# Performance work log

Hardware: AMD Instinct MI355X
Metric: run time of the kernel (lower is better)

The kernel has to match this reference:

```python
import jax, jax.numpy as jnp
import numpy as np

N_NODES = 100000
N_EDGES = 6400000
HID = 32


def setup_inputs() -> dict:
    key = jax.random.key(0)
    ks = jax.random.split(key, 24)
    inp = {
        "x_G": jax.random.normal(ks[0], (N_NODES, 1), dtype=jnp.float32),
        "edge_index_G": jax.random.randint(ks[1], (2, N_EDGES), 0, N_NODES, dtype=jnp.int32),
        "x_H": jax.random.normal(ks[2], (N_NODES, 1), dtype=jnp.float32),
        "edge_index_H": jax.random.randint(ks[3], (2, N_EDGES), 0, N_NODES, dtype=jnp.int32),
    }
    ki = 4
    for i in range(3):
        d_in = 1 if i == 0 else HID
        inp[f"W1_{i}"] = jax.random.normal(ks[ki], (d_in, HID), dtype=jnp.float32) / np.sqrt(d_in); ki += 1
        inp[f"b1_{i}"] = jnp.zeros((HID,), dtype=jnp.float32)
        inp[f"W2_{i}"] = jax.random.normal(ks[ki], (HID, HID), dtype=jnp.float32) / np.sqrt(HID); ki += 1
        inp[f"b2_{i}"] = jnp.zeros((HID,), dtype=jnp.float32)
    inp["Wc1"] = jax.random.normal(ks[ki], (2 * HID, HID), dtype=jnp.float32) / np.sqrt(2 * HID); ki += 1
    inp["bc1"] = jnp.zeros((HID,), dtype=jnp.float32)
    inp["Wc2"] = jax.random.normal(ks[ki], (HID, 1), dtype=jnp.float32) / np.sqrt(HID); ki += 1
    inp["bc2"] = jnp.zeros((1,), dtype=jnp.float32)
    return inp


def _encode(x, edge_index, layers):
    n = x.shape[0]
    src, dst = edge_index[0], edge_index[1]
    for (W1, b1, W2, b2) in layers:
        # GIN aggregation: sum of neighbor messages scattered to targets; eps = 0
        agg = jax.ops.segment_sum(x[src], dst, num_segments=n)  # [N, d]
        h = x + agg  # (1 + eps) * x + agg with eps = 0
        h = jax.nn.relu(h @ W1 + b1) @ W2 + b2  # GIN MLP
        x = jax.nn.relu(h)  # outer F.relu in encode loop
    return jnp.sum(x, axis=0, keepdims=True)  # global_add_pool, single graph -> [1, HID]


def reference(x_G, edge_index_G, x_H, edge_index_H,
              W1_0, b1_0, W2_0, b2_0,
              W1_1, b1_1, W2_1, b2_1,
              W1_2, b1_2, W2_2, b2_2,
              Wc1, bc1, Wc2, bc2):
    layers = [(W1_0, b1_0, W2_0, b2_0),
              (W1_1, b1_1, W2_1, b2_1),
              (W1_2, b1_2, W2_2, b2_2)]
    h_G = _encode(x_G, edge_index_G, layers)
    h_H = _encode(x_H, edge_index_H, layers)
    combined = jnp.concatenate([h_G, h_H], axis=1)  # [1, 2*HID]
    out = jax.nn.relu(combined @ Wc1 + bc1) @ Wc2 + bc2
    return jax.nn.sigmoid(out)
```

## Files before the change

### kernel.cpp

```cpp
#include <hip/hip_runtime.h>
#include <hip/hip_bf16.h>
#include <math.h>
#include <string.h>

#define HID 32
#define PSHIFT 8
#define NPB (1 << PSHIFT)
#define MAXP 512
#define SLOTS 17408
#define SBITS 3
#define SBINS (1 << SBITS)
#define NBINS (NPB * SBINS)
#define GS 32
#define HS_ROWS 32
#define COLBUF 3072
#define COLBUF0 6144
#define EPB 16384
typedef unsigned short u16;
typedef unsigned char u8;

__device__ inline float e42f(unsigned b) {
    unsigned u = (b & 0x7fu) << 20;
    float f; memcpy(&f, &u, 4);
    return f * 0x1p120f;
}
__device__ inline unsigned f2e4(float f) {
    f = fminf(f, 448.f);
    float y = f * 0x1p-120f;
    unsigned r; memcpy(&r, &y, 4);
    r = r + 0x7FFFFu + ((r >> 20) & 1u);
    return (r >> 20) & 0x7fu;
}
__device__ inline void acc_e4(float* a, unsigned w) {
    a[0] += e42f(w);
    a[1] += e42f(w >> 8);
    a[2] += e42f(w >> 16);
    a[3] += e42f(w >> 24);
}

__global__ void zero_kernel(float* __restrict__ p, int n) {
    int i = blockIdx.x * blockDim.x + threadIdx.x;
    if (i < n) p[i] = 0.f;
}
__global__ void init_gcur(int* __restrict__ gcur, int P) {
    int b = blockIdx.x * blockDim.x + threadIdx.x;
    if (b < P) gcur[b * GS] = b * SLOTS;
}

__global__ void partition_edges(const int* __restrict__ src, const int* __restrict__ dst,
                                int* __restrict__ gcur, unsigned* __restrict__ staged,
                                int E, int P) {
    __shared__ int hc[4][MAXP];
    __shared__ int hbase[MAXP];
    __shared__ int cur[MAXP];
    __shared__ int run[MAXP];
    __shared__ unsigned sortedv[4096];
    __shared__ u16 bktid[4096];
    __shared__ int wsums[4];
    __shared__ int sTotal;
    int t = threadIdx.x, wid = t >> 6, lane = t & 63;
    for (int i = t; i < 4 * MAXP; i += 256) (&hc[0][0])[i] = 0;
    __syncthreads();

    int base = blockIdx.x * EPB;

    {
        int cbase = base + wid * 4096;
#pragma unroll
        for (int k = 0; k < 16; k++) {
            int e = cbase + k * 256 + lane * 4;
            int4 D;
            if (e + 3 < E) {
                D = *(const int4*)(dst + e);
            } else {
                int d0[4];
                for (int j = 0; j < 4; j++) d0[j] = (e + j < E) ? dst[e + j] : -1;
                D = make_int4(d0[0], d0[1], d0[2], d0[3]);
            }
            if (D.x >= 0) atomicAdd(&hc[wid][D.x >> PSHIFT], 1);
            if (D.y >= 0) atomicAdd(&hc[wid][D.y >> PSHIFT], 1);
            if (D.z >= 0) atomicAdd(&hc[wid][D.z >> PSHIFT], 1);
            if (D.w >= 0) atomicAdd(&hc[wid][D.w >> PSHIFT], 1);
        }
    }
    __syncthreads();

    int b0 = 2 * t, b1 = 2 * t + 1;
    int tot0 = 0, tot1 = 0;
    if (b0 < P) tot0 = hc[0][b0] + hc[1][b0] + hc[2][b0] + hc[3][b0];
    if (b1 < P) tot1 = hc[0][b1] + hc[1][b1] + hc[2][b1] + hc[3][b1];
    if (b0 < P && tot0) run[b0] = atomicAdd(&gcur[b0 * GS], tot0);
    if (b1 < P && tot1) run[b1] = atomicAdd(&gcur[b1 * GS], tot1);

    for (int c = 0; c < 4; c++) {
        int t0 = (b0 < P) ? hc[c][b0] : 0;
        int t1 = (b1 < P) ? hc[c][b1] : 0;
        int s = t0 + t1;
        int incl = s;
#pragma unroll
        for (int off = 1; off < 64; off <<= 1) {
            int u = __shfl_up(incl, off, 64);
            if (lane >= off) incl += u;
        }
        if (lane == 63) wsums[wid] = incl;
        __syncthreads();
        int woff = 0;
#pragma unroll
        for (int w = 0; w < 4; w++) if (w < wid) woff += wsums[w];
        int excl = woff + incl - s;
        if (b0 < P) { hbase[b0] = excl;      cur[b0] = excl; }
        if (b1 < P) { hbase[b1] = excl + t0; cur[b1] = excl + t0; }
        if (t == 255) sTotal = excl + s;
        __syncthreads();

#pragma unroll
        for (int r = 0; r < 4; r++) {
            int e = base + c * 4096 + r * 1024 + t * 4;
            int4 S4, D4;
            if (e + 3 < E) {
                S4 = *(const int4*)(src + e);
                D4 = *(const int4*)(dst + e);
            } else {
                int s0[4], d0[4];
                for (int j = 0; j < 4; j++) {
                    int ee = e + j;
                    s0[j] = (ee < E) ? src[ee] : -1;
                    d0[j] = (ee < E) ? dst[ee] : -1;
                }
                S4 = make_int4(s0[0], s0[1], s0[2], s0[3]);
                D4 = make_int4(d0[0], d0[1], d0[2], d0[3]);
            }
            int ss[4] = { S4.x, S4.y, S4.z, S4.w };
            int dd[4] = { D4.x, D4.y, D4.z, D4.w };
#pragma unroll
            for (int j = 0; j < 4; j++) {
                int d = dd[j];
                if (d >= 0) {
                    int bk = d >> PSHIFT;
                    int pos = atomicAdd(&cur[bk], 1);
                    sortedv[pos] = ((unsigned)(d & (NPB - 1)) << 17) | (unsigned)ss[j];
                    bktid[pos]   = (u16)bk;
                }
            }
        }
        __syncthreads();

        int total = sTotal;
        for (int i = t; i < total; i += 256) {
            int bk = bktid[i];
            int addr = run[bk] + (i - hbase[bk]);
            if (addr < (bk + 1) * SLOTS)
                staged[addr] = sortedv[i];
        }
        __syncthreads();

        if (c < 3) {
            if (b0 < P && t0) run[b0] += t0;
            if (b1 < P && t1) run[b1] += t1;
        }
    }
}

__global__ void scan_buckets(const int* __restrict__ gcur, int* __restrict__ colbase,
                             int* __restrict__ rowptr, int P, int N) {
    __shared__ int wsums[4];
    int t = threadIdx.x, wid = t >> 6, lane = t & 63;
    int b0 = 2 * t, b1 = 2 * t + 1;
    int c0 = 0, c1 = 0;
    if (b0 < P) { c0 = gcur[b0 * GS] - b0 * SLOTS; if (c0 > SLOTS) c0 = SLOTS; }
    if (b1 < P) { c1 = gcur[b1 * GS] - b1 * SLOTS; if (c1 > SLOTS) c1 = SLOTS; }
    int s = c0 + c1;
    int incl = s;
#pragma unroll
    for (int off = 1; off < 64; off <<= 1) {
        int u = __shfl_up(incl, off, 64);
        if (lane >= off) incl += u;
    }
    if (lane == 63) wsums[wid] = incl;
    __syncthreads();
    int woff = 0;
#pragma unroll
    for (int w = 0; w < 4; w++) if (w < wid) woff += wsums[w];
    int excl = woff + incl - s;
    if (b0 < P) colbase[b0] = excl;
    if (b1 < P) colbase[b1] = excl + c0;
    if (t == 255) {
        colbase[P] = excl + s;
        rowptr[N]  = excl + s;
    }
}

__global__ void sort_bucket(const unsigned* __restrict__ staged, const int* __restrict__ gcur,
                            const int* __restrict__ colbase,
                            int* __restrict__ rowptr, int* __restrict__ col, int N) {
    __shared__ int cnt[NBINS];
    __shared__ int wsum[4];
    __shared__ int sorted[SLOTS];
    int b = blockIdx.x;
    int t = threadIdx.x;
    int lane = t & 63, wid = t >> 6;
    int sBeg = b * SLOTS;
    int sEnd = gcur[b * GS]; if (sEnd > sBeg + SLOTS) sEnd = sBeg + SLOTS;
    int total = sEnd - sBeg;
    int colStart = colbase[b];
    int nodeBase = b << PSHIFT;

    for (int i = t; i < NBINS; i += 256) cnt[i] = 0;
    __syncthreads();
    for (int i = sBeg + t; i < sEnd; i += 256) {
        unsigned w = staged[i];
        int key = (int)((w >> 17) << SBITS) | (int)((w & 0x1FFFFu) >> 14);
        atomicAdd(&cnt[key], 1);
    }
    __syncthreads();

    int loc[SBINS]; int tot = 0;
#pragma unroll
    for (int k = 0; k < SBINS; k++) { loc[k] = tot; tot += cnt[(t << SBITS) + k]; }
    int incl = tot;
#pragma unroll
    for (int off = 1; off < 64; off <<= 1) {
        int u = __shfl_up(incl, off, 64);
        if (lane >= off) incl += u;
    }
    if (lane == 63) wsum[wid] = incl;
    __syncthreads();
    int woff = 0;
#pragma unroll
    for (int w = 0; w < 4; w++) if (w < wid) woff += wsum[w];
    int excl = woff + incl - tot;
    int node = nodeBase + t;
    if (node < N) rowptr[node] = colStart + excl;
#pragma unroll
    for (int k = 0; k < SBINS; k++) cnt[(t << SBITS) + k] = excl + loc[k];
    __syncthreads();

    for (int i = sBeg + t; i < sEnd; i += 256) {
        unsigned w = staged[i];
        int key = (int)((w >> 17) << SBITS) | (int)((w & 0x1FFFFu) >> 14);
        int pos = atomicAdd(&cnt[key], 1);
        sorted[pos] = (int)(w & 0x1FFFFu);
    }
    __syncthreads();
    for (int i = t; i < total; i += 256)
        col[colStart + i] = sorted[i];
}

__global__ void mlp0_fused(const int* __restrict__ rowptr, const int* __restrict__ col,
                           const float* __restrict__ x0,
                           const float* __restrict__ W1, const float* __restrict__ b1,
                           const float* __restrict__ W2, const float* __restrict__ b2,
                           u8* __restrict__ out, int n) {
    __shared__ float sW1[HID], sb1[HID], sW2[HID * HID], sb2[HID];
    __shared__ int colbuf[COLBUF0];
    int t = threadIdx.x;
    if (t < HID) { sW1[t] = W1[t]; sb1[t] = b1[t]; sb2[t] = b2[t]; }
    for (int i = t; i < HID * HID; i += blockDim.x) sW2[i] = W2[i];

    int firstNode = blockIdx.x * 64;
    int lastNode  = firstNode + 64; if (lastNode > n) lastNode = n;
    int blockStart = (firstNode < n) ? rowptr[firstNode] : 0;
    int blockEnd   = (firstNode < n) ? rowptr[lastNode] : 0;
    int stagedCnt = blockEnd - blockStart; if (stagedCnt > COLBUF0) stagedCnt = COLBUF0;
    for (int i = t; i < stagedCnt; i += 256) colbuf[i] = col[blockStart + i];
    __syncthreads();

    int node = firstNode + (t >> 2);
    int q    = t & 3;
    int lane = t & 63;
    int base = lane & ~3;
    bool active = node < n;

    float s = 0.f;
    if (active) {
        int beg = rowptr[node], end = rowptr[node + 1];
        int jSplit = blockStart + stagedCnt; if (jSplit > end) jSplit = end;
        int j = beg + q;
        for (; j + 12 < jSplit; j += 16) {
            int c0 = colbuf[j - blockStart];
            int c1 = colbuf[j + 4 - blockStart];
            int c2 = colbuf[j + 8 - blockStart];
            int c3 = colbuf[j + 12 - blockStart];
            s += x0[c0]; s += x0[c1]; s += x0[c2]; s += x0[c3];
        }
        for (; j < jSplit; j += 4) s += x0[colbuf[j - blockStart]];
        for (; j < end; j += 4) s += x0[col[j]];
    }
    s += __shfl_xor(s, 1, 64);
    s += __shfl_xor(s, 2, 64);
    float v = active ? (x0[node] + s) : 0.f;

    float h[8];
#pragma unroll
    for (int i = 0; i < 8; i++) h[i] = fmaxf(fmaf(v, sW1[q * 8 + i], sb1[q * 8 + i]), 0.f);
    float o[8];
#pragma unroll
    for (int i = 0; i < 8; i++) o[i] = sb2[q * 8 + i];
#pragma unroll
    for (int k = 0; k < HID; k++) {
        float hk = __shfl(h[k & 7], base | (k >> 3), 64);
#pragma unroll
        for (int i = 0; i < 8; i++) o[i] = fmaf(hk, sW2[k * HID + q * 8 + i], o[i]);
    }
    if (active) {
        unsigned w0 = f2e4(fmaxf(o[0], 0.f)) | (f2e4(fmaxf(o[1], 0.f)) << 8)
                    | (f2e4(fmaxf(o[2], 0.f)) << 16) | (f2e4(fmaxf(o[3], 0.f)) << 24);
        unsigned w1 = f2e4(fmaxf(o[4], 0.f)) | (f2e4(fmaxf(o[5], 0.f)) << 8)
                    | (f2e4(fmaxf(o[6], 0.f)) << 16) | (f2e4(fmaxf(o[7], 0.f)) << 24);
        uint2 pk = make_uint2(w0, w1);
        *(uint2*)(out + ((size_t)node << 5) + (q << 3)) = pk;
    }
}

template <bool REDUCE>
__global__ void mlp_fused(const int* __restrict__ rowptr, const int* __restrict__ col,
                          const u8* __restrict__ xin,
                          const float* __restrict__ W1, const float* __restrict__ b1,
                          const float* __restrict__ W2, const float* __restrict__ b2,
                          u8* __restrict__ xout, float* __restrict__ hsum, int n) {
    __shared__ float sW1[HID * HID], sb1[HID], sW2[HID * HID], sb2[HID];
    __shared__ int colbuf[COLBUF];
    __shared__ float red[4][HID];
    int t = threadIdx.x;
    for (int i = t; i < HID * HID; i += blockDim.x) { sW1[i] = W1[i]; sW2[i] = W2[i]; }
    if (t < HID) { sb1[t] = b1[t]; sb2[t] = b2[t]; }

    int firstNode = blockIdx.x * 32;
    int lastNode  = firstNode + 32; if (lastNode > n) lastNode = n;
    int blockStart = (firstNode < n) ? rowptr[firstNode] : 0;
    int blockEnd   = (firstNode < n) ? rowptr[lastNode] : 0;
    int stagedCnt = blockEnd - blockStart; if (stagedCnt > COLBUF) stagedCnt = COLBUF;
    for (int i = t; i < stagedCnt; i += 256) colbuf[i] = col[blockStart + i];
    __syncthreads();

    int node = firstNode + (t >> 3);
    int q    = t & 7;
    int lane = t & 63;
    int base = lane & ~7;
    bool active = node < n;

    float va[4];
#pragma unroll
    for (int i = 0; i < 4; i++) va[i] = 0.f;
    if (active) {
        int beg = rowptr[node], end = rowptr[node + 1];
        const u8* xq = xin + (q << 2);
        float a0[4], a1[4], a2[4], a3[4];
#pragma unroll
        for (int i = 0; i < 4; i++) a0[i] = a1[i] = a2[i] = a3[i] = 0.f;
        {
            unsigned w = *(const unsigned*)(xq + ((size_t)node << 5));
            acc_e4(a0, w);
        }
        int jSplit = blockStart + stagedCnt; if (jSplit > end) jSplit = end;
        int j = beg;
        for (; j + 8 <= jSplit; j += 8) {
            int lj = j - blockStart;
            int c0 = colbuf[lj+0], c1 = colbuf[lj+1], c2 = colbuf[lj+2], c3 = colbuf[lj+3];
            int c4 = colbuf[lj+4], c5 = colbuf[lj+5], c6 = colbuf[lj+6], c7 = colbuf[lj+7];
            unsigned w0 = *(const unsigned*)(xq + ((size_t)c0 << 5));
            unsigned w1 = *(const unsigned*)(xq + ((size_t)c1 << 5));
            unsigned w2 = *(const unsigned*)(xq + ((size_t)c2 << 5));
            unsigned w3 = *(const unsigned*)(xq + ((size_t)c3 << 5));
            unsigned w4 = *(const unsigned*)(xq + ((size_t)c4 << 5));
            unsigned w5 = *(const unsigned*)(xq + ((size_t)c5 << 5));
            unsigned w6 = *(const unsigned*)(xq + ((size_t)c6 << 5));
            unsigned w7 = *(const unsigned*)(xq + ((size_t)c7 << 5));
            acc_e4(a0, w0); acc_e4(a1, w1); acc_e4(a2, w2); acc_e4(a3, w3);
            acc_e4(a0, w4); acc_e4(a1, w5); acc_e4(a2, w6); acc_e4(a3, w7);
        }
        for (; j < jSplit; j++) {
            unsigned w = *(const unsigned*)(xq + ((size_t)colbuf[j - blockStart] << 5));
            acc_e4(a0, w);
        }
        for (; j < end; j++) {
            unsigned w = *(const unsigned*)(xq + ((size_t)col[j] << 5));
            acc_e4(a0, w);
        }
#pragma unroll
        for (int i = 0; i < 4; i++) va[i] = (a0[i] + a1[i]) + (a2[i] + a3[i]);
    }

    float h[4];
#pragma unroll
    for (int i = 0; i < 4; i++) h[i] = sb1[q * 4 + i];
#pragma unroll
    for (int k = 0; k < HID; k++) {
        float vk = __shfl(va[k & 3], base | (k >> 2), 64);
#pragma unroll
        for (int i = 0; i < 4; i++) h[i] = fmaf(vk, sW1[k * HID + q * 4 + i], h[i]);
    }
#pragma unroll
    for (int i = 0; i < 4; i++) h[i] = fmaxf(h[i], 0.f);

    float o[4];
#pragma unroll
    for (int i = 0; i < 4; i++) o[i] = sb2[q * 4 + i];
#pragma unroll
    for (int k = 0; k < HID; k++) {
        float hk = __shfl(h[k & 3], base | (k >> 2), 64);
#pragma unroll
        for (int i = 0; i < 4; i++) o[i] = fmaf(hk, sW2[k * HID + q * 4 + i], o[i]);
    }
#pragma unroll
    for (int i = 0; i < 4; i++) o[i] = fmaxf(o[i], 0.f);

    if (REDUCE) {
        if (!active) {
#pragma unroll
            for (int i = 0; i < 4; i++) o[i] = 0.f;
        }
#pragma unroll
        for (int i = 0; i < 4; i++) {
            float v = o[i];
            v += __shfl_xor(v, 8, 64);
            v += __shfl_xor(v, 16, 64);
            v += __shfl_xor(v, 32, 64);
            o[i] = v;
        }
        int wid = t >> 6;
        if (lane < 8) {
#pragma unroll
            for (int i = 0; i < 4; i++) red[wid][lane * 4 + i] = o[i];
        }
        __syncthreads();
        if (t < HID) {
            float s = red[0][t] + red[1][t] + red[2][t] + red[3][t];
            atomicAdd(&hsum[(blockIdx.x & (HS_ROWS - 1)) * (2 * HID) + t], s);
        }
    } else if (active) {
        unsigned pw = f2e4(o[0]) | (f2e4(o[1]) << 8) | (f2e4(o[2]) << 16) | (f2e4(o[3]) << 24);
        *(unsigned*)(xout + ((size_t)node << 5) + (q << 2)) = pw;
    }
}

__global__ void head_kernel(const float* __restrict__ hsumP,
                            const float* __restrict__ Wc1, const float* __restrict__ bc1,
                            const float* __restrict__ Wc2, const float* __restrict__ bc2,
                            float* __restrict__ out) {
    __shared__ float hs[2 * HID];
    int t = threadIdx.x;
    if (t < 2 * HID) {
        float s = 0.f;
        for (int r = 0; r < HS_ROWS; r++) s += hsumP[r * (2 * HID) + t];
        hs[t] = s;
    }
    __syncthreads();
    float val = 0.f;
    if (t < HID) {
        float acc = bc1[t];
        for (int i = 0; i < 2 * HID; i++) acc = fmaf(hs[i], Wc1[i * HID + t], acc);
        val = fmaxf(acc, 0.f) * Wc2[t];
    }
    for (int off = 32; off >= 1; off >>= 1) val += __shfl_xor(val, off, 64);
    if (t == 0) out[0] = 1.f / (1.f + expf(-(val + bc2[0])));
}

extern "C" void kernel_launch(void* const* d_in, const int* in_sizes, int n_in,
                              void* d_out, int out_size, void* d_ws, size_t ws_size,
                              hipStream_t stream) {
    const float* xg[2] = { (const float*)d_in[0], (const float*)d_in[2] };
    const int*   eg[2] = { (const int*)d_in[1],   (const int*)d_in[3] };
    const float* W1[3] = { (const float*)d_in[4], (const float*)d_in[8],  (const float*)d_in[12] };
    const float* b1[3] = { (const float*)d_in[5], (const float*)d_in[9],  (const float*)d_in[13] };
    const float* W2[3] = { (const float*)d_in[6], (const float*)d_in[10], (const float*)d_in[14] };
    const float* b2[3] = { (const float*)d_in[7], (const float*)d_in[11], (const float*)d_in[15] };
    const float* Wc1 = (const float*)d_in[16];
    const float* bc1 = (const float*)d_in[17];
    const float* Wc2 = (const float*)d_in[18];
    const float* bc2 = (const float*)d_in[19];

    const int N = in_sizes[0];
    const int E = in_sizes[1] / 2;
    const int P = (N + NPB - 1) >> PSHIFT;

    u8*       B0      = (u8*)d_ws;
    u8*       B1      = B0 + (size_t)N * 32;
    float*    hsumP   = (float*)(B1 + (size_t)N * 32);
    int*      rowptr  = (int*)(hsumP + HS_ROWS * 2 * HID);
    int*      col     = rowptr + (N + 1);
    int*      colbase = col + (size_t)E;
    int*      gcur    = colbase + (P + 1);
    unsigned* staged  = (unsigned*)(gcur + (size_t)P * GS);

    const int TB = 256;
    dim3 blk(TB);
    int gE16k = (E + EPB - 1) / EPB;
    int gN64 = (N + 63) / 64;
    int gN8  = (N + 31) / 32;
    int gP   = (P + TB - 1) / TB;

    zero_kernel<<<(HS_ROWS * 2 * HID + 255) / 256, 256, 0, stream>>>(hsumP, HS_ROWS * 2 * HID);

    for (int g = 0; g < 2; g++) {
        const float* x0  = xg[g];
        const int*   src = eg[g];
        const int*   dst = src + E;

        init_gcur<<<gP, blk, 0, stream>>>(gcur, P);
        partition_edges<<<gE16k, blk, 0, stream>>>(src, dst, gcur, staged, E, P);
        scan_buckets<<<1, blk, 0, stream>>>(gcur, colbase, rowptr, P, N);
        sort_bucket<<<P, blk, 0, stream>>>(staged, gcur, colbase, rowptr, col, N);

        mlp0_fused<<<gN64, blk, 0, stream>>>(rowptr, col, x0, W1[0], b1[0], W2[0], b2[0], B0, N);

        mlp_fused<false><<<gN8, blk, 0, stream>>>(rowptr, col, B0, W1[1], b1[1], W2[1], b2[1],
                                                  B1, nullptr, N);

        mlp_fused<true><<<gN8, blk, 0, stream>>>(rowptr, col, B1, W1[2], b1[2], W2[2], b2[2],
                                                 nullptr, hsumP + g * HID, N);
    }

    head_kernel<<<1, 64, 0, stream>>>(hsumP, Wc1, bc1, Wc2, bc2, (float*)d_out);
}
```

Before: 586.6 us.

## Use hardware FP8 convert builtins and halve edges per partition block

Replaces the software E4M3 encode/decode bit manipulation with the packed hardware conversion builtins (cvt_pk_f32_fp8 / cvt_pk_fp8_f32) when available, which shortens the inner gather-accumulate loops and output packing. Separately, it halves the edges handled per partition block (each wave-pair now shares one sorting pass, two passes instead of four), doubling the partition grid size. The hardware converter may round and handle saturation or NaN slightly differently from the software path, and more blocks means more global atomics on the bucket cursors.

```diff
diff --git a/kernel.cpp b/kernel.cpp
--- a/kernel.cpp
+++ b/kernel.cpp
@@ -15,16 +15,17 @@
 #define HS_ROWS 32
 #define COLBUF 3072
 #define COLBUF0 6144
-#define EPB 16384
+#define EPB 8192
 typedef unsigned short u16;
 typedef unsigned char u8;
-
-__device__ inline float e42f(unsigned b) {
+typedef float f32x2 __attribute__((ext_vector_type(2)));
+
+__device__ inline float e42f_sw(unsigned b) {
     unsigned u = (b & 0x7fu) << 20;
     float f; memcpy(&f, &u, 4);
     return f * 0x1p120f;
 }
-__device__ inline unsigned f2e4(float f) {
+__device__ inline unsigned f2e4_sw(float f) {
     f = fminf(f, 448.f);
     float y = f * 0x1p-120f;
     unsigned r; memcpy(&r, &y, 4);
@@ -32,10 +33,27 @@
     return (r >> 20) & 0x7fu;
 }
 __device__ inline void acc_e4(float* a, unsigned w) {
-    a[0] += e42f(w);
-    a[1] += e42f(w >> 8);
-    a[2] += e42f(w >> 16);
-    a[3] += e42f(w >> 24);
+#if __has_builtin(__builtin_amdgcn_cvt_pk_f32_fp8)
+    f32x2 lo = __builtin_amdgcn_cvt_pk_f32_fp8(w, false);
+    f32x2 hi = __builtin_amdgcn_cvt_pk_f32_fp8(w, true);
+    a[0] += lo.x; a[1] += lo.y; a[2] += hi.x; a[3] += hi.y;
+#else
+    a[0] += e42f_sw(w);
+    a[1] += e42f_sw(w >> 8);
+    a[2] += e42f_sw(w >> 16);
+    a[3] += e42f_sw(w >> 24);
+#endif
+}
+__device__ inline unsigned pack_e4(float o0, float o1, float o2, float o3) {
+#if __has_builtin(__builtin_amdgcn_cvt_pk_fp8_f32)
+    unsigned pw = (unsigned)__builtin_amdgcn_cvt_pk_fp8_f32(
+        fminf(o0, 448.f), fminf(o1, 448.f), 0, false);
+    pw = (unsigned)__builtin_amdgcn_cvt_pk_fp8_f32(
+        fminf(o2, 448.f), fminf(o3, 448.f), pw, true);
+    return pw;
+#else
+    return f2e4_sw(o0) | (f2e4_sw(o1) << 8) | (f2e4_sw(o2) << 16) | (f2e4_sw(o3) << 24);
+#endif
 }
 
 __global__ void zero_kernel(float* __restrict__ p, int n) {
@@ -65,9 +83,9 @@
     int base = blockIdx.x * EPB;
 
     {
-        int cbase = base + wid * 4096;
-#pragma unroll
-        for (int k = 0; k < 16; k++) {
+        int cbase = base + wid * 2048;
+#pragma unroll
+        for (int k = 0; k < 8; k++) {
             int e = cbase + k * 256 + lane * 4;
             int4 D;
             if (e + 3 < E) {
@@ -92,9 +110,9 @@
     if (b0 < P && tot0) run[b0] = atomicAdd(&gcur[b0 * GS], tot0);
     if (b1 < P && tot1) run[b1] = atomicAdd(&gcur[b1 * GS], tot1);
 
-    for (int c = 0; c < 4; c++) {
-        int t0 = (b0 < P) ? hc[c][b0] : 0;
-        int t1 = (b1 < P) ? hc[c][b1] : 0;
+    for (int c = 0; c < 2; c++) {
+        int t0 = (b0 < P) ? (hc[2 * c][b0] + hc[2 * c + 1][b0]) : 0;
+        int t1 = (b1 < P) ? (hc[2 * c][b1] + hc[2 * c + 1][b1]) : 0;
         int s = t0 + t1;
         int incl = s;
 #pragma unroll
@@ -154,7 +172,7 @@
         }
         __syncthreads();
 
-        if (c < 3) {
+        if (c == 0) {
             if (b0 < P && t0) run[b0] += t0;
             if (b1 < P && t1) run[b1] += t1;
         }
@@ -303,10 +321,10 @@
         for (int i = 0; i < 8; i++) o[i] = fmaf(hk, sW2[k * HID + q * 8 + i], o[i]);
     }
     if (active) {
-        unsigned w0 = f2e4(fmaxf(o[0], 0.f)) | (f2e4(fmaxf(o[1], 0.f)) << 8)
-                    | (f2e4(fmaxf(o[2], 0.f)) << 16) | (f2e4(fmaxf(o[3], 0.f)) << 24);
-        unsigned w1 = f2e4(fmaxf(o[4], 0.f)) | (f2e4(fmaxf(o[5], 0.f)) << 8)
-                    | (f2e4(fmaxf(o[6], 0.f)) << 16) | (f2e4(fmaxf(o[7], 0.f)) << 24);
+        unsigned w0 = pack_e4(fmaxf(o[0], 0.f), fmaxf(o[1], 0.f),
+                              fmaxf(o[2], 0.f), fmaxf(o[3], 0.f));
+        unsigned w1 = pack_e4(fmaxf(o[4], 0.f), fmaxf(o[5], 0.f),
+                              fmaxf(o[6], 0.f), fmaxf(o[7], 0.f));
         uint2 pk = make_uint2(w0, w1);
         *(uint2*)(out + ((size_t)node << 5) + (q << 3)) = pk;
     }
@@ -429,7 +447,7 @@
             atomicAdd(&hsum[(blockIdx.x & (HS_ROWS - 1)) * (2 * HID) + t], s);
         }
     } else if (active) {
-        unsigned pw = f2e4(o[0]) | (f2e4(o[1]) << 8) | (f2e4(o[2]) << 16) | (f2e4(o[3]) << 24);
+        unsigned pw = pack_e4(o[0], o[1], o[2], o[3]);
         *(unsigned*)(xout + ((size_t)node << 5) + (q << 2)) = pw;
     }
 }
@@ -485,7 +503,7 @@
 
     const int TB = 256;
     dim3 blk(TB);
-    int gE16k = (E + EPB - 1) / EPB;
+    int gE8k = (E + EPB - 1) / EPB;
     int gN64 = (N + 63) / 64;
     int gN8  = (N + 31) / 32;
     int gP   = (P + TB - 1) / TB;
@@ -498,7 +516,7 @@
         const int*   dst = src + E;
 
         init_gcur<<<gP, blk, 0, stream>>>(gcur, P);
-        partition_edges<<<gE16k, blk, 0, stream>>>(src, dst, gcur, staged, E, P);
+        partition_edges<<<gE8k, blk, 0, stream>>>(src, dst, gcur, staged, E, P);
         scan_buckets<<<1, blk, 0, stream>>>(gcur, colbase, rowptr, P, N);
         sort_bucket<<<P, blk, 0, stream>>>(staged, gcur, colbase, rowptr, col, N);
 
```

After: 580.0 us. No clear change (-1.1%).
